# Optimization experiments

Hardware: AMD Instinct MI355X
Metric: run time of the kernel (lower is better)

## Reference

```python
import jax, jax.numpy as jnp
import numpy as np

B, S, D = 4, 1024, 1024
H, DK, DH = 16, 64, 64  # num_heads, key_size, head_size
NEG = 1e12


def setup_inputs() -> dict:
    key = jax.random.key(0)
    ks = jax.random.split(key, 16)
    scale = 0.02
    inp = {
        'q': jax.random.normal(ks[0], (B, S, D), jnp.float32),
        'k': jax.random.normal(ks[1], (B, S, D), jnp.float32),
        'v': jax.random.normal(ks[2], (B, S, D), jnp.float32),
        'v_mask': jax.random.randint(ks[3], (B, S), 0, 2, jnp.int32),
        'q_mask': jax.random.randint(ks[4], (B, S), 0, 2, jnp.int32),
        # causal attention mask (float, 1 = keep)
        'a_mask': jnp.tril(jnp.ones((S, S), jnp.float32))[None, None, :, :],
        'Wq': jax.random.normal(ks[5], (D, H * DK), jnp.float32) * scale,
        'bq': jnp.zeros((H * DK,), jnp.float32),
        'Wk': jax.random.normal(ks[6], (D, H * DK), jnp.float32) * scale,
        'bk': jnp.zeros((H * DK,), jnp.float32),
        'Wv': jax.random.normal(ks[7], (D, H * DH), jnp.float32) * scale,
        'bv': jnp.zeros((H * DH,), jnp.float32),
        'Wo': jax.random.normal(ks[8], (H * DH, H * DH), jnp.float32) * scale,
        'bo': jnp.zeros((H * DH,), jnp.float32),
    }
    return inp


def reference(q, k, v, v_mask, q_mask, a_mask, Wq, bq, Wk, bk, Wv, bv, Wo, bo):
    b, sq, _ = q.shape
    sk = k.shape[1]
    qw = (jnp.einsum('bsd,de->bse', q, Wq) + bq).reshape(b, sq, H, DK)
    kw = (jnp.einsum('bsd,de->bse', k, Wk) + bk).reshape(b, sk, H, DK)
    vw = (jnp.einsum('bsd,de->bse', v, Wv) + bv).reshape(b, sk, H, DH)
    # scores [b, h, sq, sk]
    a = jnp.einsum('bjhd,bkhd->bhjk', qw, kw) / jnp.sqrt(jnp.float32(DK))
    vm = v_mask.astype(jnp.float32)  # [b, sk]
    a = a - (1.0 - vm)[:, None, None, :] * NEG  # sequence_masking mode='add'
    a = a - (1.0 - a_mask) * NEG                # attention mask
    p = jax.nn.softmax(a, axis=-1)
    o = jnp.einsum('bhjk,bkhd->bjhd', p, vw).reshape(b, sq, H * DH)
    o = jnp.einsum('bse,ef->bsf', o, Wo) + bo
    qm = q_mask.astype(jnp.float32)
    o = o * qm[:, :, None]  # sequence_masking mode='mul'
    return o
```

## Files before the change

### kernel.cpp

```cpp
#include <hip/hip_runtime.h>
#include <cstdint>
#include <cstddef>

typedef unsigned short u16;
using short8 = __attribute__((ext_vector_type(8))) short;
using f32x4  = __attribute__((ext_vector_type(4))) float;

constexpr int Sc = 1024;
constexpr float PEN = 60.0f;

__device__ __forceinline__ u16 f2bf(float f) {
  union { float f; uint32_t u; } v; v.f = f;
  return (u16)((v.u + 0x7fffu + ((v.u >> 16) & 1u)) >> 16);
}

__device__ __forceinline__ void gload_lds16(const u16* g, u16* l) {
  __builtin_amdgcn_global_load_lds(
      (const __attribute__((address_space(1))) uint32_t*)g,
      (__attribute__((address_space(3))) uint32_t*)l, 16, 0, 0);
}

__device__ __forceinline__ f32x4 mfma16(short8 a, short8 b, f32x4 c) {
  return __builtin_amdgcn_mfma_f32_16x16x32_bf16(a, b, c, 0, 0, 0);
}

__global__ __launch_bounds__(256) void prep(
    const float* __restrict__ q, const float* __restrict__ k,
    const float* __restrict__ v, u16* __restrict__ qb, u16* __restrict__ kb,
    u16* __restrict__ vb, const float* __restrict__ W0,
    const float* __restrict__ W1, const float* __restrict__ W2,
    const float* __restrict__ W3, u16* __restrict__ D0, u16* __restrict__ D1,
    u16* __restrict__ D2, u16* __restrict__ D3) {
  const int y = blockIdx.y;
  if (y < 3) {
    const float* src = y == 0 ? q : y == 1 ? k : v;
    u16* dst = y == 0 ? qb : y == 1 ? kb : vb;
    int i = blockIdx.x * 256 + threadIdx.x;
    float4 a = ((const float4*)src)[2 * i];
    float4 b = ((const float4*)src)[2 * i + 1];
    u16 t[8] = {f2bf(a.x), f2bf(a.y), f2bf(a.z), f2bf(a.w),
                f2bf(b.x), f2bf(b.y), f2bf(b.z), f2bf(b.w)};
    ((uint4*)dst)[i] = *(const uint4*)t;
  } else {
    if (blockIdx.x >= 1024) return;
    const int z = y - 3;
    const float* W = z == 0 ? W0 : z == 1 ? W1 : z == 2 ? W2 : W3;
    u16* WT = z == 0 ? D0 : z == 1 ? D1 : z == 2 ? D2 : D3;
    __shared__ float t[32][33];
    int bx = (blockIdx.x & 31) * 32, by = (blockIdx.x >> 5) * 32;
    int tx = threadIdx.x & 31, ty = threadIdx.x >> 5;
    for (int i = 0; i < 32; i += 8)
      t[ty + i][tx] = W[(size_t)(by + ty + i) * 1024 + bx + tx];
    __syncthreads();
    for (int i = 0; i < 32; i += 8)
      WT[(size_t)(bx + ty + i) * 1024 + by + tx] = f2bf(t[tx][ty + i]);
  }
}

__global__ __launch_bounds__(256, 6) void gemm_qkv(
    const u16* __restrict__ qb, const u16* __restrict__ kb,
    const u16* __restrict__ vb, const u16* __restrict__ BT,
    const float* __restrict__ bq, const float* __restrict__ bk,
    const float* __restrict__ bv, u16* __restrict__ QW, u16* __restrict__ KW,
    u16* __restrict__ VTg) {
  const int bid = blockIdx.x;
  const int xcd = bid & 7, local = bid >> 3;
  const int mp = local & 3, nbi = local >> 2;
  const int m0 = (xcd * 4 + mp) * 128, n0 = nbi * 64;
  const int seg = nbi >> 4;
  const u16* A    = seg == 0 ? qb : seg == 1 ? kb : vb;
  const float* bias = seg == 0 ? bq : seg == 1 ? bk : bv;

  __shared__ u16 As0[128 * 32], As1[128 * 32];
  __shared__ u16 Bs0[64 * 32], Bs1[64 * 32];

  const int t = threadIdx.x, w = t >> 6, lane = t & 63;
  const int q4 = lane >> 4, lm = lane & 15;
  const int wm = (w >> 1) * 64, wn = (w & 1) * 32;
  const int srow = lane >> 2, p = lane & 3;
  const int cf = q4 ^ ((lm >> 2) & 3);

  const int rbA0 = (w * 2) * 16, rbA1 = (w * 2 + 1) * 16, rbB = w * 16;
  const int rowA0 = rbA0 + srow, rowA1 = rbA1 + srow, rowB = rbB + srow;
  const int cA0 = p ^ ((rowA0 >> 2) & 3), cA1 = p ^ ((rowA1 >> 2) & 3);
  const int cB = p ^ ((rowB >> 2) & 3);
  const u16* pa0 = &A[(size_t)(m0 + rowA0) * 1024 + cA0 * 8];
  const u16* pa1 = &A[(size_t)(m0 + rowA1) * 1024 + cA1 * 8];
  const u16* pb  = &BT[(size_t)(n0 + rowB) * 1024 + cB * 8];

  f32x4 acc[4][2] = {};

  auto stage = [&](u16* as, u16* bs) {
    gload_lds16(pa0, as + rbA0 * 32);
    gload_lds16(pa1, as + rbA1 * 32);
    gload_lds16(pb, bs + rbB * 32);
    pa0 += 32; pa1 += 32; pb += 32;
  };
  auto compute = [&](const u16* as, const u16* bs) {
    short8 af[4], bf[2];
    for (int mi = 0; mi < 4; ++mi)
      af[mi] = *(const short8*)&as[(wm + mi * 16 + lm) * 32 + cf * 8];
    for (int ni = 0; ni < 2; ++ni)
      bf[ni] = *(const short8*)&bs[(wn + ni * 16 + lm) * 32 + cf * 8];
    for (int mi = 0; mi < 4; ++mi)
      for (int ni = 0; ni < 2; ++ni)
        acc[mi][ni] = mfma16(af[mi], bf[ni], acc[mi][ni]);
  };

  stage(As0, Bs0);
  for (int it = 0; it < 16; ++it) {
    __syncthreads();
    stage(As1, Bs1);
    compute(As0, Bs0);
    __syncthreads();
    if (it < 15) stage(As0, Bs0);
    compute(As1, Bs1);
  }

  if (seg < 2) {
    u16* C = seg == 0 ? QW : KW;
    for (int mi = 0; mi < 4; ++mi)
      for (int ni = 0; ni < 2; ++ni)
        for (int r = 0; r < 4; ++r) {
          int row = m0 + wm + mi * 16 + q4 * 4 + r;
          int col = (n0 + wn + ni * 16 + lm) & 1023;
          C[(size_t)row * 1024 + col] = f2bf(acc[mi][ni][r] + bias[col]);
        }
  } else {
    for (int mi = 0; mi < 4; ++mi)
      for (int ni = 0; ni < 2; ++ni) {
        int row0 = m0 + wm + mi * 16 + q4 * 4;
        int col = (n0 + wn + ni * 16 + lm) & 1023;
        float bv4 = bias[col];
        u16 o4[4];
        for (int r = 0; r < 4; ++r) o4[r] = f2bf(acc[mi][ni][r] + bv4);
        *(uint2*)&VTg[(size_t)col * 4096 + row0] = *(const uint2*)o4;
      }
  }
}

__global__ __launch_bounds__(256, 4) void gemm_out(
    const u16* __restrict__ A, const u16* __restrict__ BT,
    const float* __restrict__ bias, const int* __restrict__ qmask,
    float* __restrict__ Cf) {
  const int bid = blockIdx.x;
  const int xcd = bid & 7, local = bid >> 3;
  const int mp = local & 7, nb = local >> 3;
  const int m0 = (xcd * 8 + mp) * 64, n0 = nb * 64;

  __shared__ u16 As0[64 * 32], As1[64 * 32];
  __shared__ u16 Bs0[64 * 32], Bs1[64 * 32];
  const int t = threadIdx.x, w = t >> 6, lane = t & 63;
  const int q4 = lane >> 4, lm = lane & 15;
  const int wm = (w >> 1) * 32, wn = (w & 1) * 32;
  const int srow = lane >> 2, p = lane & 3;
  const int cf = q4 ^ ((lm >> 2) & 3);

  const int rb = w * 16;
  const int rowS = rb + srow;
  const int cS = p ^ ((rowS >> 2) & 3);
  const u16* pa = &A[(size_t)(m0 + rowS) * 1024 + cS * 8];
  const u16* pb = &BT[(size_t)(n0 + rowS) * 1024 + cS * 8];

  f32x4 acc[2][2] = {};

  auto stage = [&](u16* as, u16* bs) {
    gload_lds16(pa, as + rb * 32);
    gload_lds16(pb, bs + rb * 32);
    pa += 32; pb += 32;
  };
  auto compute = [&](const u16* as, const u16* bs) {
    short8 af[2], bf[2];
    for (int mi = 0; mi < 2; ++mi)
      af[mi] = *(const short8*)&as[(wm + mi * 16 + lm) * 32 + cf * 8];
    for (int ni = 0; ni < 2; ++ni)
      bf[ni] = *(const short8*)&bs[(wn + ni * 16 + lm) * 32 + cf * 8];
    for (int mi = 0; mi < 2; ++mi)
      for (int ni = 0; ni < 2; ++ni)
        acc[mi][ni] = mfma16(af[mi], bf[ni], acc[mi][ni]);
  };

  stage(As0, Bs0);
  for (int it = 0; it < 16; ++it) {
    __syncthreads();
    stage(As1, Bs1);
    compute(As0, Bs0);
    __syncthreads();
    if (it < 15) stage(As0, Bs0);
    compute(As1, Bs1);
  }

  for (int mi = 0; mi < 2; ++mi)
    for (int ni = 0; ni < 2; ++ni)
      for (int r = 0; r < 4; ++r) {
        int row = m0 + wm + mi * 16 + q4 * 4 + r;
        int col = n0 + wn + ni * 16 + lm;
        Cf[(size_t)row * 1024 + col] =
            (acc[mi][ni][r] + bias[col]) * (float)qmask[row];
      }
}

__global__ __launch_bounds__(256) void attn(
    const u16* __restrict__ QW, const u16* __restrict__ KW,
    const u16* __restrict__ VTg, const int* __restrict__ vmask,
    u16* __restrict__ O) {
  const int bid = blockIdx.x;
  const int xcd = bid & 7, local = bid >> 3;
  const int pair = xcd * 8 + (local & 7);
  const int b = pair >> 4, h = pair & 15;
  const int bx = local >> 3;
  const int qta = bx, qtb = 15 - bx;
  const int t = threadIdx.x, w = t >> 6, lane = t & 63;
  const int q4 = lane >> 4, lm = lane & 15;

  __shared__ u16 Ks[2][64 * 64];
  __shared__ u16 VTs[2][64 * 64];
  __shared__ u16 P[4][16 * 88];
  __shared__ float penv[1024];
  __shared__ int anyf[2];

  if (t < 2) anyf[t] = 0;
  {
    int4 vm = ((const int4*)(vmask + b * 1024))[t];
    penv[4 * t + 0] = (1.f - (float)vm.x) * PEN;
    penv[4 * t + 1] = (1.f - (float)vm.y) * PEN;
    penv[4 * t + 2] = (1.f - (float)vm.z) * PEN;
    penv[4 * t + 3] = (1.f - (float)vm.w) * PEN;
  }
  __syncthreads();
  {
    int any_a = 0, any_b = 0;
    for (int i = t; i <= qtb * 64; i += 256) {
      int un = (penv[i] == 0.f);
      if (i <= qta * 64) any_a |= un;
      any_b |= un;
    }
    if (any_a) atomicOr(&anyf[0], 1);
    if (any_b) atomicOr(&anyf[1], 1);
  }
  __syncthreads();
  const int extA = !anyf[0], extB = !anyf[1];
  const int kend = (extA || extB) ? 15 : qtb;

  short8 qf[2][2];
  for (int s = 0; s < 2; ++s) {
    int qt = s ? qtb : qta;
    const u16* qp = &QW[(size_t)(b * Sc + qt * 64 + w * 16 + lm) * 1024 + h * 64];
    qf[s][0] = *(const short8*)&qp[q4 * 8];
    qf[s][1] = *(const short8*)&qp[32 + q4 * 8];
    for (int fi = 0; fi < 2; ++fi)
      for (int i = 0; i < 8; ++i) {
        u16 x = (u16)qf[s][fi][i];
        int e = (x >> 7) & 0xff;
        qf[s][fi][i] = (short)(e > 3 ? (u16)(x - 0x180) : (u16)(x & 0x8000));
      }
  }

  float l_run[2][4] = {};
  f32x4 oacc[2][4] = {};

  const int r0 = lane >> 3, pos = lane & 7, ch = pos ^ r0;
  auto stage = [&](int kt, int buf) {
    for (int j = 0; j < 2; ++j) {
      int issue = w * 2 + j;
      int row = issue * 8 + r0;
      gload_lds16(&KW[(size_t)(b * Sc + kt * 64 + row) * 1024 + h * 64 + ch * 8],
                  &Ks[buf][issue * 512]);
      gload_lds16(&VTg[(size_t)(h * 64 + row) * 4096 + b * Sc + kt * 64 + ch * 8],
                  &VTs[buf][issue * 512]);
    }
  };

  auto strip_tile = [&](int s, int kt, int mode, int buf) {
    const int qt = s ? qtb : qta;
    const int qrow0 = qt * 64 + w * 16 + q4 * 4;
    f32x4 sacc[4] = {};
    for (int ni = 0; ni < 4; ++ni) {
      int row = ni * 16 + lm;
      short8 kf0 = *(const short8*)&Ks[buf][row * 64 + ((q4 ^ (lm & 7)) * 8)];
      short8 kf1 = *(const short8*)&Ks[buf][row * 64 + (((4 + q4) ^ (lm & 7)) * 8)];
      sacc[ni] = mfma16(qf[s][0], kf0, sacc[ni]);
      sacc[ni] = mfma16(qf[s][1], kf1, sacc[ni]);
    }
    u16* Pw = &P[w][0];
    for (int ni = 0; ni < 4; ++ni) {
      int key = kt * 64 + ni * 16 + lm;
      float pen = penv[key];
      if (mode == 2) pen += PEN;
      for (int r = 0; r < 4; ++r) {
        float x = sacc[ni][r] - pen;
        if (mode == 1 && key > qrow0 + r) x -= PEN;
        float pv = __expf(x);
        l_run[s][r] += pv;
        Pw[(q4 * 4 + r) * 88 + ni * 16 + lm] = f2bf(pv);
      }
    }
    short8 pf0 = *(const short8*)&Pw[lm * 88 + q4 * 8];
    short8 pf1 = *(const short8*)&Pw[lm * 88 + 32 + q4 * 8];
    for (int ni = 0; ni < 4; ++ni) {
      int row = ni * 16 + lm;
      short8 vf0 = *(const short8*)&VTs[buf][row * 64 + ((q4 ^ (lm & 7)) * 8)];
      short8 vf1 = *(const short8*)&VTs[buf][row * 64 + (((4 + q4) ^ (lm & 7)) * 8)];
      oacc[s][ni] = mfma16(pf0, vf0, oacc[s][ni]);
      oacc[s][ni] = mfma16(pf1, vf1, oacc[s][ni]);
    }
  };

  stage(0, 0);
  int cur = 0;
  for (int kt = 0; kt <= kend; ++kt) {
    __syncthreads();
    if (kt < kend) stage(kt + 1, cur ^ 1);
    if (kt <= qta) strip_tile(0, kt, kt == qta ? 1 : 0, cur);
    else if (extA) strip_tile(0, kt, 2, cur);
    if (kt <= qtb) strip_tile(1, kt, kt == qtb ? 1 : 0, cur);
    else if (extB) strip_tile(1, kt, 2, cur);
    cur ^= 1;
  }

  for (int s = 0; s < 2; ++s) {
    int qt = s ? qtb : qta;
    for (int r = 0; r < 4; ++r) {
      float l = l_run[s][r];
      for (int off = 1; off < 16; off <<= 1) l += __shfl_xor(l, off, 64);
      l_run[s][r] = 1.0f / l;
    }
    for (int ni = 0; ni < 4; ++ni)
      for (int r = 0; r < 4; ++r) {
        int row = b * Sc + qt * 64 + w * 16 + q4 * 4 + r;
        O[(size_t)row * 1024 + h * 64 + ni * 16 + lm] =
            f2bf(oacc[s][ni][r] * l_run[s][r]);
      }
  }
}

extern "C" void kernel_launch(void* const* d_in, const int* in_sizes, int n_in,
                              void* d_out, int out_size, void* d_ws, size_t ws_size,
                              hipStream_t stream) {
  (void)in_sizes; (void)n_in; (void)out_size; (void)ws_size;
  const float* q  = (const float*)d_in[0];
  const float* k  = (const float*)d_in[1];
  const float* v  = (const float*)d_in[2];
  const int* vmask = (const int*)d_in[3];
  const int* qmask = (const int*)d_in[4];
  const float* Wq = (const float*)d_in[6];
  const float* bq = (const float*)d_in[7];
  const float* Wk = (const float*)d_in[8];
  const float* bk = (const float*)d_in[9];
  const float* Wv = (const float*)d_in[10];
  const float* bv = (const float*)d_in[11];
  const float* Wo = (const float*)d_in[12];
  const float* bo = (const float*)d_in[13];

  char* ws = (char*)d_ws;
  u16* WT3 = (u16*)ws;
  u16* WoT = (u16*)(ws + 6291456);
  u16* QW  = (u16*)(ws + 8388608);
  u16* KW  = (u16*)(ws + 16777216);
  u16* VTg = (u16*)(ws + 25165824);
  u16* Oat = (u16*)(ws + 33554432);
  u16* qb = (u16*)d_out;
  u16* kb = (u16*)d_out + 4194304;
  u16* vb = Oat;

  dim3 tb(256);
  prep<<<dim3(2048, 7), tb, 0, stream>>>(q, k, v, qb, kb, vb, Wq, Wk, Wv, Wo,
                                         WT3, WT3 + 1048576, WT3 + 2097152,
                                         WoT);
  gemm_qkv<<<dim3(1536), tb, 0, stream>>>(qb, kb, vb, WT3, bq, bk, bv, QW, KW,
                                          VTg);
  attn<<<dim3(512), tb, 0, stream>>>(QW, KW, VTg, vmask, Oat);
  gemm_out<<<dim3(1024), tb, 0, stream>>>(Oat, WoT, bo, qmask, (float*)d_out);
}
```

Before: 224.3 us.

## Double K-tile depth in QKV GEMM and move masked-prefix rows to separate fixup kernel

The QKV GEMM now stages 64-wide K slices instead of 32, halving the number of loop iterations and barriers, with a new 8-way XOR swizzle, and it drops the occupancy hint from launch bounds. The attention kernel no longer scans the value mask or runs extra key tiles for rows whose visible keys are all masked. Those leading rows, up to the first unmasked key, are handled by a new per-(batch, head) fixup kernel that recomputes them exactly with scalar loops. This adds an extra launch and serial scalar work proportional to the masked prefix length, in exchange for a simpler, shorter main attention loop.

```diff
diff --git a/kernel.cpp b/kernel.cpp
--- a/kernel.cpp
+++ b/kernel.cpp
@@ -12,6 +12,11 @@
 __device__ __forceinline__ u16 f2bf(float f) {
   union { float f; uint32_t u; } v; v.f = f;
   return (u16)((v.u + 0x7fffu + ((v.u >> 16) & 1u)) >> 16);
+}
+
+__device__ __forceinline__ float bf2f(u16 x) {
+  union { uint32_t u; float f; } v; v.u = (uint32_t)x << 16;
+  return v.f;
 }
 
 __device__ __forceinline__ void gload_lds16(const u16* g, u16* l) {
@@ -57,7 +62,7 @@
   }
 }
 
-__global__ __launch_bounds__(256, 6) void gemm_qkv(
+__global__ __launch_bounds__(256) void gemm_qkv(
     const u16* __restrict__ qb, const u16* __restrict__ kb,
     const u16* __restrict__ vb, const u16* __restrict__ BT,
     const float* __restrict__ bq, const float* __restrict__ bk,
@@ -71,49 +76,58 @@
   const u16* A    = seg == 0 ? qb : seg == 1 ? kb : vb;
   const float* bias = seg == 0 ? bq : seg == 1 ? bk : bv;
 
-  __shared__ u16 As0[128 * 32], As1[128 * 32];
-  __shared__ u16 Bs0[64 * 32], Bs1[64 * 32];
+  __shared__ u16 As0[128 * 64], As1[128 * 64];
+  __shared__ u16 Bs0[64 * 64], Bs1[64 * 64];
 
   const int t = threadIdx.x, w = t >> 6, lane = t & 63;
   const int q4 = lane >> 4, lm = lane & 15;
   const int wm = (w >> 1) * 64, wn = (w & 1) * 32;
-  const int srow = lane >> 2, p = lane & 3;
-  const int cf = q4 ^ ((lm >> 2) & 3);
-
-  const int rbA0 = (w * 2) * 16, rbA1 = (w * 2 + 1) * 16, rbB = w * 16;
-  const int rowA0 = rbA0 + srow, rowA1 = rbA1 + srow, rowB = rbB + srow;
-  const int cA0 = p ^ ((rowA0 >> 2) & 3), cA1 = p ^ ((rowA1 >> 2) & 3);
-  const int cB = p ^ ((rowB >> 2) & 3);
-  const u16* pa0 = &A[(size_t)(m0 + rowA0) * 1024 + cA0 * 8];
-  const u16* pa1 = &A[(size_t)(m0 + rowA1) * 1024 + cA1 * 8];
-  const u16* pb  = &BT[(size_t)(n0 + rowB) * 1024 + cB * 8];
+  const int r8i = lane >> 3, pos = lane & 7;
+
+  const u16* paP[4];
+  const u16* pbP[2];
+  for (int j = 0; j < 4; ++j) {
+    int row = (w * 4 + j) * 8 + r8i;
+    paP[j] = &A[(size_t)(m0 + row) * 1024 + (pos ^ r8i) * 8];
+  }
+  for (int j = 0; j < 2; ++j) {
+    int row = (w * 2 + j) * 8 + r8i;
+    pbP[j] = &BT[(size_t)(n0 + row) * 1024 + (pos ^ r8i) * 8];
+  }
 
   f32x4 acc[4][2] = {};
 
   auto stage = [&](u16* as, u16* bs) {
-    gload_lds16(pa0, as + rbA0 * 32);
-    gload_lds16(pa1, as + rbA1 * 32);
-    gload_lds16(pb, bs + rbB * 32);
-    pa0 += 32; pa1 += 32; pb += 32;
+    for (int j = 0; j < 4; ++j) {
+      gload_lds16(paP[j], as + (w * 4 + j) * 512);
+      paP[j] += 64;
+    }
+    for (int j = 0; j < 2; ++j) {
+      gload_lds16(pbP[j], bs + (w * 2 + j) * 512);
+      pbP[j] += 64;
+    }
   };
   auto compute = [&](const u16* as, const u16* bs) {
-    short8 af[4], bf[2];
-    for (int mi = 0; mi < 4; ++mi)
-      af[mi] = *(const short8*)&as[(wm + mi * 16 + lm) * 32 + cf * 8];
-    for (int ni = 0; ni < 2; ++ni)
-      bf[ni] = *(const short8*)&bs[(wn + ni * 16 + lm) * 32 + cf * 8];
-    for (int mi = 0; mi < 4; ++mi)
+    for (int kk = 0; kk < 2; ++kk) {
+      const int co = ((kk * 4 + q4) ^ (lm & 7)) * 8;
+      short8 af[4], bf[2];
+      for (int mi = 0; mi < 4; ++mi)
+        af[mi] = *(const short8*)&as[(wm + mi * 16 + lm) * 64 + co];
       for (int ni = 0; ni < 2; ++ni)
-        acc[mi][ni] = mfma16(af[mi], bf[ni], acc[mi][ni]);
+        bf[ni] = *(const short8*)&bs[(wn + ni * 16 + lm) * 64 + co];
+      for (int mi = 0; mi < 4; ++mi)
+        for (int ni = 0; ni < 2; ++ni)
+          acc[mi][ni] = mfma16(af[mi], bf[ni], acc[mi][ni]);
+    }
   };
 
   stage(As0, Bs0);
-  for (int it = 0; it < 16; ++it) {
+  for (int it = 0; it < 8; ++it) {
     __syncthreads();
     stage(As1, Bs1);
     compute(As0, Bs0);
     __syncthreads();
-    if (it < 15) stage(As0, Bs0);
+    if (it < 7) stage(As0, Bs0);
     compute(As1, Bs1);
   }
 
@@ -217,9 +231,7 @@
   __shared__ u16 VTs[2][64 * 64];
   __shared__ u16 P[4][16 * 88];
   __shared__ float penv[1024];
-  __shared__ int anyf[2];
-
-  if (t < 2) anyf[t] = 0;
+
   {
     int4 vm = ((const int4*)(vmask + b * 1024))[t];
     penv[4 * t + 0] = (1.f - (float)vm.x) * PEN;
@@ -228,19 +240,6 @@
     penv[4 * t + 3] = (1.f - (float)vm.w) * PEN;
   }
   __syncthreads();
-  {
-    int any_a = 0, any_b = 0;
-    for (int i = t; i <= qtb * 64; i += 256) {
-      int un = (penv[i] == 0.f);
-      if (i <= qta * 64) any_a |= un;
-      any_b |= un;
-    }
-    if (any_a) atomicOr(&anyf[0], 1);
-    if (any_b) atomicOr(&anyf[1], 1);
-  }
-  __syncthreads();
-  const int extA = !anyf[0], extB = !anyf[1];
-  const int kend = (extA || extB) ? 15 : qtb;
 
   short8 qf[2][2];
   for (int s = 0; s < 2; ++s) {
@@ -286,7 +285,6 @@
     for (int ni = 0; ni < 4; ++ni) {
       int key = kt * 64 + ni * 16 + lm;
       float pen = penv[key];
-      if (mode == 2) pen += PEN;
       for (int r = 0; r < 4; ++r) {
         float x = sacc[ni][r] - pen;
         if (mode == 1 && key > qrow0 + r) x -= PEN;
@@ -308,13 +306,11 @@
 
   stage(0, 0);
   int cur = 0;
-  for (int kt = 0; kt <= kend; ++kt) {
-    __syncthreads();
-    if (kt < kend) stage(kt + 1, cur ^ 1);
+  for (int kt = 0; kt <= qtb; ++kt) {
+    __syncthreads();
+    if (kt < qtb) stage(kt + 1, cur ^ 1);
     if (kt <= qta) strip_tile(0, kt, kt == qta ? 1 : 0, cur);
-    else if (extA) strip_tile(0, kt, 2, cur);
-    if (kt <= qtb) strip_tile(1, kt, kt == qtb ? 1 : 0, cur);
-    else if (extB) strip_tile(1, kt, 2, cur);
+    strip_tile(1, kt, kt == qtb ? 1 : 0, cur);
     cur ^= 1;
   }
 
@@ -331,6 +327,61 @@
         O[(size_t)row * 1024 + h * 64 + ni * 16 + lm] =
             f2bf(oacc[s][ni][r] * l_run[s][r]);
       }
+  }
+}
+
+__global__ __launch_bounds__(256) void attn_fix(
+    const u16* __restrict__ QW, const u16* __restrict__ KW,
+    const u16* __restrict__ VTg, const int* __restrict__ vmask,
+    u16* __restrict__ O) {
+  const int b = blockIdx.x >> 4, h = blockIdx.x & 15;
+  const int t = threadIdx.x;
+  __shared__ int lzs;
+  __shared__ float pbuf[1024];
+  __shared__ float qs[64];
+  __shared__ float sred;
+  __shared__ float ored[64];
+  if (t == 0) lzs = 1024;
+  __syncthreads();
+  for (int j = t; j < 1024; j += 256)
+    if (vmask[b * 1024 + j]) atomicMin(&lzs, j);
+  __syncthreads();
+  const int Lz = lzs;
+  if (Lz == 0) return;
+  for (int r = 0; r < Lz; ++r) {
+    if (t < 64) {
+      qs[t] = bf2f(QW[(size_t)(b * 1024 + r) * 1024 + h * 64 + t]);
+      ored[t] = 0.f;
+    }
+    if (t == 0) sred = 0.f;
+    __syncthreads();
+    float lsum = 0.f;
+    for (int jj = 0; jj < 4; ++jj) {
+      int j = t * 4 + jj;
+      float p = 0.f;
+      if (j <= r || vmask[b * 1024 + j]) {
+        const u16* kp = &KW[(size_t)(b * 1024 + j) * 1024 + h * 64];
+        float s = 0.f;
+        for (int d = 0; d < 64; ++d) s += qs[d] * bf2f(kp[d]);
+        p = __expf(s * 0.125f);
+      }
+      pbuf[j] = p;
+      lsum += p;
+    }
+    atomicAdd(&sred, lsum);
+    __syncthreads();
+    const float inv = 1.0f / sred;
+    {
+      int d = t & 63, c = t >> 6;
+      const u16* vp = &VTg[(size_t)(h * 64 + d) * 4096 + b * 1024 + c * 256];
+      float acc = 0.f;
+      for (int j = 0; j < 256; ++j) acc += pbuf[c * 256 + j] * bf2f(vp[j]);
+      atomicAdd(&ored[d], acc);
+    }
+    __syncthreads();
+    if (t < 64)
+      O[(size_t)(b * 1024 + r) * 1024 + h * 64 + t] = f2bf(ored[t] * inv);
+    __syncthreads();
   }
 }
 
@@ -370,5 +421,6 @@
   gemm_qkv<<<dim3(1536), tb, 0, stream>>>(qb, kb, vb, WT3, bq, bk, bv, QW, KW,
                                           VTg);
   attn<<<dim3(512), tb, 0, stream>>>(QW, KW, VTg, vmask, Oat);
+  attn_fix<<<dim3(64), tb, 0, stream>>>(QW, KW, VTg, vmask, Oat);
   gemm_out<<<dim3(1024), tb, 0, stream>>>(Oat, WoT, bo, qmask, (float*)d_out);
 }
```

Result: slower. 230.6 us (+2.8%).
